# Performance work log

Hardware: AMD Instinct MI355X
Metric: run time of the kernel (lower is better)

## Reference

```python
import jax, jax.numpy as jnp
import numpy as np

L, N, D, K = 8, 1024, 2048, 4096

def setup_inputs() -> dict:
    key = jax.random.key(0)
    k1, k2 = jax.random.split(key)
    x = jax.random.normal(k1, (L, N, D), dtype=jnp.float32)
    centroids = jax.random.normal(k2, (L, K, D), dtype=jnp.float32)
    return {"x": x, "centroids": centroids}

def reference(x, centroids):
    # Euclidean distance of every row of x[l] to every centroid in centroids[l]:
    # ||a-b||^2 = ||a||^2 - 2 a.b + ||b||^2, computed as batched GEMM (one per layer,
    # fused into a single einsum) instead of the original per-row Python loop.
    x2 = jnp.sum(x * x, axis=-1)                        # [L, N]
    c2 = jnp.sum(centroids * centroids, axis=-1)        # [L, K]
    xc = jnp.einsum('lnd,lkd->lnk', x, centroids)       # [L, N, K]
    d2 = x2[:, :, None] - 2.0 * xc + c2[:, None, :]
    return jnp.sqrt(jnp.maximum(d2, 1e-12))             # [L, N, K]
```

## Files before the change

### kernel.cpp

```cpp
#include <hip/hip_runtime.h>
#include <hip/hip_bf16.h>


#define L_DIM 8
#define N_DIM 1024
#define D_DIM 2048
#define K_DIM 4096

typedef __bf16 bf16x8 __attribute__((ext_vector_type(8)));
typedef float floatx4 __attribute__((ext_vector_type(4)));


__device__ __forceinline__ unsigned short f2bf_rne(float f) {
    unsigned u = __float_as_uint(f);
    unsigned r = (u + 0x7FFFu + ((u >> 16) & 1u)) >> 16;
    return (unsigned short)r;
}

__device__ __forceinline__ void lds_cp16(const unsigned short* g, unsigned short* l) {
    __builtin_amdgcn_global_load_lds(
        (const __attribute__((address_space(1))) void*)g,
        (__attribute__((address_space(3))) void*)l,
        16, 0, 0);
}

__global__ __launch_bounds__(256) void prep_kernel(const float* __restrict__ src,
                                                   unsigned short* __restrict__ dst,
                                                   float* __restrict__ norms) {
    const int wave = threadIdx.x >> 6;
    const int lane = threadIdx.x & 63;
    const int row  = blockIdx.x * 4 + wave;
    const size_t rb = (size_t)row * D_DIM;

    float s = 0.f;
    #pragma unroll
    for (int p = 0; p < 4; p++) {
        const size_t base = rb + (size_t)p * 512 + (size_t)lane * 8;
        float4 f0 = *(const float4*)(src + base);
        float4 f1 = *(const float4*)(src + base + 4);

        union { unsigned short us[8]; int4 v; } pk;
        pk.us[0] = f2bf_rne(f0.x); pk.us[1] = f2bf_rne(f0.y);
        pk.us[2] = f2bf_rne(f0.z); pk.us[3] = f2bf_rne(f0.w);
        pk.us[4] = f2bf_rne(f1.x); pk.us[5] = f2bf_rne(f1.y);
        pk.us[6] = f2bf_rne(f1.z); pk.us[7] = f2bf_rne(f1.w);
        *(int4*)(dst + base) = pk.v;

        s += f0.x*f0.x + f0.y*f0.y + f0.z*f0.z + f0.w*f0.w
           + f1.x*f1.x + f1.y*f1.y + f1.z*f1.z + f1.w*f1.w;
    }
    #pragma unroll
    for (int off = 32; off > 0; off >>= 1) s += __shfl_down(s, off, 64);
    if (lane == 0) norms[row] = s;
}

__global__ __launch_bounds__(256) void gemm_mfma(const unsigned short* __restrict__ xb,
                                                 const unsigned short* __restrict__ cb,
                                                 const float* __restrict__ x2,
                                                 const float* __restrict__ c2,
                                                 float* __restrict__ out) {
    __shared__ unsigned short As[128 * 64];
    __shared__ unsigned short Bs[128 * 64];

    const int l  = blockIdx.z;
    const int nb = blockIdx.y;
    const int kb = blockIdx.x;

    const unsigned short* xA = xb + (size_t)l * N_DIM * D_DIM + (size_t)(nb * 128) * D_DIM;
    const unsigned short* cB = cb + (size_t)l * K_DIM * D_DIM + (size_t)(kb * 128) * D_DIM;

    const int t    = threadIdx.x;
    const int wave = t >> 6;
    const int lane = t & 63;
    const int quad = lane >> 4;
    const int lr   = lane & 15;
    const int sw   = lr & 7;
    const int wr   = (wave >> 1) * 64;
    const int wc   = (wave & 1) * 64;

    floatx4 acc[4][4];
    const floatx4 zero = {0.f, 0.f, 0.f, 0.f};
    #pragma unroll
    for (int i = 0; i < 4; i++)
        #pragma unroll
        for (int j = 0; j < 4; j++) acc[i][j] = zero;

    for (int d0 = 0; d0 < D_DIM; d0 += 64) {
        #pragma unroll
        for (int i = 0; i < 4; i++) {
            const int id  = i * 256 + t;
            const int row = id >> 3;
            const int cc  = id & 7;
            const int gcc = cc ^ (row & 7);
            const int ldsbase = (i * 256 + wave * 64) * 8;
            lds_cp16(xA + (size_t)row * D_DIM + d0 + gcc * 8, &As[ldsbase]);
            lds_cp16(cB + (size_t)row * D_DIM + d0 + gcc * 8, &Bs[ldsbase]);
        }
        __syncthreads();

        #pragma unroll
        for (int ks = 0; ks < 2; ks++) {
            bf16x8 a[4], b[4];
            #pragma unroll
            for (int im = 0; im < 4; im++)
                a[im] = *(const bf16x8*)&As[(wr + im * 16 + lr) * 64 + ((ks * 4 + quad) ^ sw) * 8];
            #pragma unroll
            for (int jn = 0; jn < 4; jn++)
                b[jn] = *(const bf16x8*)&Bs[(wc + jn * 16 + lr) * 64 + ((ks * 4 + quad) ^ sw) * 8];
            #pragma unroll
            for (int im = 0; im < 4; im++)
                #pragma unroll
                for (int jn = 0; jn < 4; jn++)
                    acc[im][jn] = __builtin_amdgcn_mfma_f32_16x16x32_bf16(
                        a[im], b[jn], acc[im][jn], 0, 0, 0);
        }
        __syncthreads();
    }

    const float* x2l = x2 + l * N_DIM + nb * 128;
    const float* c2l = c2 + l * K_DIM + kb * 128;
    float* outl = out + (size_t)l * N_DIM * K_DIM + (size_t)(nb * 128) * K_DIM + kb * 128;

    #pragma unroll
    for (int im = 0; im < 4; im++) {
        const int rbase = wr + im * 16 + quad * 4;
        #pragma unroll
        for (int jn = 0; jn < 4; jn++) {
            const int col = wc + jn * 16 + lr;
            const float c2v = c2l[col];
            #pragma unroll
            for (int r = 0; r < 4; r++) {
                const int row = rbase + r;
                const float d2 = x2l[row] - 2.0f * acc[im][jn][r] + c2v;
                outl[(size_t)row * K_DIM + col] = sqrtf(fmaxf(d2, 1e-12f));
            }
        }
    }
}

__global__ __launch_bounds__(256) void fallback_dist(const float* __restrict__ x,
                                                     const float* __restrict__ c,
                                                     float* __restrict__ out) {
    __shared__ float As[64][33];
    __shared__ float Bs[64][33];
    const int l = blockIdx.z, nb = blockIdx.y, kb = blockIdx.x;
    const float* xA = x + (size_t)l * N_DIM * D_DIM + (size_t)(nb * 64) * D_DIM;
    const float* cB = c + (size_t)l * K_DIM * D_DIM + (size_t)(kb * 64) * D_DIM;
    const int t = threadIdx.x;
    const int tr = t >> 4, tc = t & 15;
    float acc[4][4] = {};
    for (int d0 = 0; d0 < D_DIM; d0 += 32) {
        #pragma unroll
        for (int i = 0; i < 8; i++) {
            const int id = i * 256 + t;
            const int r = id >> 5, cc = id & 31;
            As[r][cc] = xA[(size_t)r * D_DIM + d0 + cc];
            Bs[r][cc] = cB[(size_t)r * D_DIM + d0 + cc];
        }
        __syncthreads();
        #pragma unroll
        for (int kk = 0; kk < 32; kk++) {
            float av[4], bv[4];
            #pragma unroll
            for (int i = 0; i < 4; i++) av[i] = As[tr * 4 + i][kk];
            #pragma unroll
            for (int j = 0; j < 4; j++) bv[j] = Bs[tc * 4 + j][kk];
            #pragma unroll
            for (int i = 0; i < 4; i++)
                #pragma unroll
                for (int j = 0; j < 4; j++) {
                    const float dxy = av[i] - bv[j];
                    acc[i][j] += dxy * dxy;
                }
        }
        __syncthreads();
    }
    float* o = out + (size_t)l * N_DIM * K_DIM + (size_t)(nb * 64) * K_DIM + kb * 64;
    #pragma unroll
    for (int i = 0; i < 4; i++)
        #pragma unroll
        for (int j = 0; j < 4; j++)
            o[(size_t)(tr * 4 + i) * K_DIM + tc * 4 + j] = sqrtf(fmaxf(acc[i][j], 1e-12f));
}

extern "C" void kernel_launch(void* const* d_in, const int* in_sizes, int n_in,
                              void* d_out, int out_size, void* d_ws, size_t ws_size,
                              hipStream_t stream) {
    const float* x = (const float*)d_in[0];
    const float* c = (const float*)d_in[1];
    float* out = (float*)d_out;

    constexpr size_t X_ELEMS = (size_t)L_DIM * N_DIM * D_DIM;
    constexpr size_t C_ELEMS = (size_t)L_DIM * K_DIM * D_DIM;
    constexpr size_t NEED = X_ELEMS * 2 + C_ELEMS * 2
                          + (size_t)L_DIM * N_DIM * 4 + (size_t)L_DIM * K_DIM * 4;

    if (ws_size >= NEED) {
        unsigned short* xb = (unsigned short*)d_ws;
        unsigned short* cb = xb + X_ELEMS;
        float* x2 = (float*)(cb + C_ELEMS);
        float* c2 = x2 + (size_t)L_DIM * N_DIM;

        prep_kernel<<<L_DIM * N_DIM / 4, 256, 0, stream>>>(x, xb, x2);
        prep_kernel<<<L_DIM * K_DIM / 4, 256, 0, stream>>>(c, cb, c2);
        gemm_mfma<<<dim3(K_DIM / 128, N_DIM / 128, L_DIM), 256, 0, stream>>>(xb, cb, x2, c2, out);
    } else {
        fallback_dist<<<dim3(K_DIM / 64, N_DIM / 64, L_DIM), 256, 0, stream>>>(x, c, out);
    }
}
```

Measured before the change: 652.6 us.

## Switch GEMM to 32x32x16 MFMA, precompute load pointers, merge prep kernels

The GEMM inner loop moves from 16x16x32 bf16 MFMA tiles (4x4 per wave) to 32x32x16 tiles (2x2 per wave). This cuts the number of LDS fragment reads per MFMA and the instruction count, and the epilogue row mapping is adjusted to match. Global-to-LDS source pointers are now computed once and advanced each iteration instead of being recomputed. The two bf16 conversion/norm kernels are merged into one launch to save a launch. The risks are different register pressure and a changed LDS bank-access pattern under the existing swizzle.

```diff
diff --git a/kernel.cpp b/kernel.cpp
--- a/kernel.cpp
+++ b/kernel.cpp
@@ -8,7 +8,7 @@
 #define K_DIM 4096
 
 typedef __bf16 bf16x8 __attribute__((ext_vector_type(8)));
-typedef float floatx4 __attribute__((ext_vector_type(4)));
+typedef float floatx16 __attribute__((ext_vector_type(16)));
 
 
 __device__ __forceinline__ unsigned short f2bf_rne(float f) {
@@ -24,14 +24,21 @@
         16, 0, 0);
 }
 
-__global__ __launch_bounds__(256) void prep_kernel(const float* __restrict__ src,
-                                                   unsigned short* __restrict__ dst,
-                                                   float* __restrict__ norms) {
+__global__ __launch_bounds__(256) void prep_all(const float* __restrict__ x,
+                                                const float* __restrict__ c,
+                                                unsigned short* __restrict__ xb,
+                                                unsigned short* __restrict__ cb,
+                                                float* __restrict__ x2,
+                                                float* __restrict__ c2) {
     const int wave = threadIdx.x >> 6;
     const int lane = threadIdx.x & 63;
-    const int row  = blockIdx.x * 4 + wave;
+    const int gw   = blockIdx.x * 4 + wave;
+
+    const float* src; unsigned short* dst; float* nrm; int row;
+    if (gw < L_DIM * N_DIM) { src = x; dst = xb; nrm = x2; row = gw; }
+    else { src = c; dst = cb; nrm = c2; row = gw - L_DIM * N_DIM; }
+
     const size_t rb = (size_t)row * D_DIM;
-
     float s = 0.f;
     #pragma unroll
     for (int p = 0; p < 4; p++) {
@@ -51,7 +58,7 @@
     }
     #pragma unroll
     for (int off = 32; off > 0; off >>= 1) s += __shfl_down(s, off, 64);
-    if (lane == 0) norms[row] = s;
+    if (lane == 0) nrm[row] = s;
 }
 
 __global__ __launch_bounds__(256) void gemm_mfma(const unsigned short* __restrict__ xb,
@@ -72,47 +79,53 @@
     const int t    = threadIdx.x;
     const int wave = t >> 6;
     const int lane = t & 63;
-    const int quad = lane >> 4;
-    const int lr   = lane & 15;
-    const int sw   = lr & 7;
+    const int l31  = lane & 31;
+    const int lh   = lane >> 5;
+    const int swz  = lane & 7;
     const int wr   = (wave >> 1) * 64;
     const int wc   = (wave & 1) * 64;
 
-    floatx4 acc[4][4];
-    const floatx4 zero = {0.f, 0.f, 0.f, 0.f};
-    #pragma unroll
-    for (int i = 0; i < 4; i++)
-        #pragma unroll
-        for (int j = 0; j < 4; j++) acc[i][j] = zero;
+    const unsigned short* pA[4];
+    const unsigned short* pB[4];
+    unsigned short* ldsA[4];
+    unsigned short* ldsB[4];
+    #pragma unroll
+    for (int i = 0; i < 4; i++) {
+        const int id  = i * 256 + t;
+        const int row = id >> 3;
+        const int cc  = id & 7;
+        const int gcc = cc ^ (row & 7);
+        pA[i] = xA + (size_t)row * D_DIM + gcc * 8;
+        pB[i] = cB + (size_t)row * D_DIM + gcc * 8;
+        ldsA[i] = &As[(i * 256 + wave * 64) * 8];
+        ldsB[i] = &Bs[(i * 256 + wave * 64) * 8];
+    }
+
+    floatx16 acc[2][2] = {};
 
     for (int d0 = 0; d0 < D_DIM; d0 += 64) {
         #pragma unroll
         for (int i = 0; i < 4; i++) {
-            const int id  = i * 256 + t;
-            const int row = id >> 3;
-            const int cc  = id & 7;
-            const int gcc = cc ^ (row & 7);
-            const int ldsbase = (i * 256 + wave * 64) * 8;
-            lds_cp16(xA + (size_t)row * D_DIM + d0 + gcc * 8, &As[ldsbase]);
-            lds_cp16(cB + (size_t)row * D_DIM + d0 + gcc * 8, &Bs[ldsbase]);
-        }
-        __syncthreads();
-
-        #pragma unroll
-        for (int ks = 0; ks < 2; ks++) {
-            bf16x8 a[4], b[4];
-            #pragma unroll
-            for (int im = 0; im < 4; im++)
-                a[im] = *(const bf16x8*)&As[(wr + im * 16 + lr) * 64 + ((ks * 4 + quad) ^ sw) * 8];
-            #pragma unroll
-            for (int jn = 0; jn < 4; jn++)
-                b[jn] = *(const bf16x8*)&Bs[(wc + jn * 16 + lr) * 64 + ((ks * 4 + quad) ^ sw) * 8];
-            #pragma unroll
-            for (int im = 0; im < 4; im++)
+            lds_cp16(pA[i], ldsA[i]);
+            lds_cp16(pB[i], ldsB[i]);
+            pA[i] += 64; pB[i] += 64;
+        }
+        __syncthreads();
+
+        #pragma unroll
+        for (int s = 0; s < 4; s++) {
+            const int co = (((s << 1) | lh) ^ swz) << 3;
+            bf16x8 a[2], b[2];
+            a[0] = *(const bf16x8*)&As[(wr +      l31) * 64 + co];
+            a[1] = *(const bf16x8*)&As[(wr + 32 + l31) * 64 + co];
+            b[0] = *(const bf16x8*)&Bs[(wc +      l31) * 64 + co];
+            b[1] = *(const bf16x8*)&Bs[(wc + 32 + l31) * 64 + co];
+            #pragma unroll
+            for (int i = 0; i < 2; i++)
                 #pragma unroll
-                for (int jn = 0; jn < 4; jn++)
-                    acc[im][jn] = __builtin_amdgcn_mfma_f32_16x16x32_bf16(
-                        a[im], b[jn], acc[im][jn], 0, 0, 0);
+                for (int j = 0; j < 2; j++)
+                    acc[i][j] = __builtin_amdgcn_mfma_f32_32x32x16_bf16(
+                        a[i], b[j], acc[i][j], 0, 0, 0);
         }
         __syncthreads();
     }
@@ -122,16 +135,15 @@
     float* outl = out + (size_t)l * N_DIM * K_DIM + (size_t)(nb * 128) * K_DIM + kb * 128;
 
     #pragma unroll
-    for (int im = 0; im < 4; im++) {
-        const int rbase = wr + im * 16 + quad * 4;
-        #pragma unroll
-        for (int jn = 0; jn < 4; jn++) {
-            const int col = wc + jn * 16 + lr;
+    for (int i = 0; i < 2; i++) {
+        #pragma unroll
+        for (int j = 0; j < 2; j++) {
+            const int col = wc + j * 32 + l31;
             const float c2v = c2l[col];
             #pragma unroll
-            for (int r = 0; r < 4; r++) {
-                const int row = rbase + r;
-                const float d2 = x2l[row] - 2.0f * acc[im][jn][r] + c2v;
+            for (int r = 0; r < 16; r++) {
+                const int row = wr + i * 32 + (r & 3) + 8 * (r >> 2) + 4 * lh;
+                const float d2 = x2l[row] - 2.0f * acc[i][j][r] + c2v;
                 outl[(size_t)row * K_DIM + col] = sqrtf(fmaxf(d2, 1e-12f));
             }
         }
@@ -201,8 +213,7 @@
         float* x2 = (float*)(cb + C_ELEMS);
         float* c2 = x2 + (size_t)L_DIM * N_DIM;
 
-        prep_kernel<<<L_DIM * N_DIM / 4, 256, 0, stream>>>(x, xb, x2);
-        prep_kernel<<<L_DIM * K_DIM / 4, 256, 0, stream>>>(c, cb, c2);
+        prep_all<<<L_DIM * (N_DIM + K_DIM) / 4, 256, 0, stream>>>(x, c, xb, cb, x2, c2);
         gemm_mfma<<<dim3(K_DIM / 128, N_DIM / 128, L_DIM), 256, 0, stream>>>(xb, cb, x2, c2, out);
     } else {
         fallback_dist<<<dim3(K_DIM / 64, N_DIM / 64, L_DIM), 256, 0, stream>>>(x, c, out);
```

New measurement: 636.4 us. 1.03x faster.
